# Kernel tuning notes

Measured on AMD Instinct MI355X. Metric: run time of the kernel, lower is better.

Reference implementation:

```python
import jax, jax.numpy as jnp
import numpy as np

B, T, N = 128, 20, 49
VOCAB, EMB, HDIM, VDIM, ATT = 10000, 512, 1024, 512, 512
LN_EPS = 1e-5


def _layer_norm(x, g, b):
    mu = x.mean(-1, keepdims=True)
    var = ((x - mu) ** 2).mean(-1, keepdims=True)
    return (x - mu) * jax.lax.rsqrt(var + LN_EPS) * g + b


def _lstm_cell(x, h, c, Wih, Whh, bih, bhh):
    gates = x @ Wih.T + h @ Whh.T + bih + bhh  # [B, 4H]
    i, f, g, o = jnp.split(gates, 4, axis=-1)  # torch LSTMCell gate order
    c_new = jax.nn.sigmoid(f) * c + jax.nn.sigmoid(i) * jnp.tanh(g)
    h_new = jax.nn.sigmoid(o) * jnp.tanh(c_new)
    return h_new, c_new


def setup_inputs() -> dict:
    key = jax.random.key(0)
    ks = jax.random.split(key, 16)
    w = lambda k, shape: (jax.random.normal(k, shape, jnp.float32) * 0.02)
    embed_W = w(ks[2], (VOCAB, EMB)).at[0].set(0.0)  # padding_idx=0 row is zeros
    return dict(
        V=jax.random.normal(ks[0], (B, N, VDIM), jnp.float32),
        y=jax.random.randint(ks[1], (B, T), 0, VOCAB),
        embed_W=embed_W,
        Vp_W=w(ks[3], (HDIM, VDIM)), Vp_b=jnp.zeros((HDIM,), jnp.float32),
        attW=w(ks[4], (ATT, HDIM)), attU=w(ks[5], (ATT, HDIM)), attv=w(ks[6], (1, ATT)),
        l1_Wih=w(ks[7], (4 * HDIM, EMB + HDIM)), l1_Whh=w(ks[8], (4 * HDIM, HDIM)),
        l1_bih=jnp.zeros((4 * HDIM,), jnp.float32), l1_bhh=jnp.zeros((4 * HDIM,), jnp.float32),
        l2_Wih=w(ks[9], (4 * HDIM, HDIM)), l2_Whh=w(ks[10], (4 * HDIM, HDIM)),
        l2_bih=jnp.zeros((4 * HDIM,), jnp.float32), l2_bhh=jnp.zeros((4 * HDIM,), jnp.float32),
        n1_g=jnp.ones((HDIM,), jnp.float32), n1_b=jnp.zeros((HDIM,), jnp.float32),
        n2_g=jnp.ones((HDIM,), jnp.float32), n2_b=jnp.zeros((HDIM,), jnp.float32),
        ih_W=w(ks[11], (HDIM, HDIM)), ih_b=jnp.zeros((HDIM,), jnp.float32),
        ic_W=w(ks[12], (HDIM, HDIM)), ic_b=jnp.zeros((HDIM,), jnp.float32),
        proj_W=w(ks[13], (EMB, HDIM)),
    )


def reference(V, y, embed_W, Vp_W, Vp_b, attW, attU, attv,
              l1_Wih, l1_Whh, l1_bih, l1_bhh,
              l2_Wih, l2_Whh, l2_bih, l2_bhh,
              n1_g, n1_b, n2_g, n2_b,
              ih_W, ih_b, ic_W, ic_b, proj_W):
    Vp = V @ Vp_W.T + Vp_b                      # [B, N, H]
    feat_mean = Vp.mean(1)                      # [B, H]
    h1 = jnp.tanh(feat_mean @ ih_W.T + ih_b)
    c1 = jnp.tanh(feat_mean @ ic_W.T + ic_b)
    h2 = jnp.zeros_like(h1)
    c2 = jnp.zeros_like(c1)

    Uv = Vp @ attU.T                            # [B, N, ATT] (hoisted out of loop)
    emb_y = embed_W[y]                          # [B, T, EMB]
    xs = jnp.swapaxes(emb_y[:, :-1], 0, 1)      # [T-1, B, EMB]

    def step(carry, x_t):
        h1, c1, h2, c2 = carry
        # additive attention (dropout is identity in eval)
        e = jnp.tanh((h2 @ attW.T)[:, None, :] + Uv) @ attv[0]   # [B, N]
        a = jax.nn.softmax(e, axis=1)
        ctx = jnp.einsum('bn,bnh->bh', a, Vp)
        h1n, c1n = _lstm_cell(jnp.concatenate([x_t, ctx], -1), h1, c1,
                              l1_Wih, l1_Whh, l1_bih, l1_bhh)
        h1n = _layer_norm(h1n, n1_g, n1_b)
        h2n, c2n = _lstm_cell(h1n, h2, c2, l2_Wih, l2_Whh, l2_bih, l2_bhh)
        h2n = _layer_norm(h2n, n2_g, n2_b)
        logit = (h2n @ proj_W.T) @ embed_W.T    # [B, VOCAB]
        return (h1n, c1n, h2n, c2n), logit

    _, logits = jax.lax.scan(step, (h1, c1, h2, c2), xs)
    return jnp.swapaxes(logits, 0, 1)           # [B, T-1, VOCAB]
```

## Files before the change

kernel.cpp:

```cpp
#include <hip/hip_runtime.h>
#include <hip/hip_bf16.h>

#define TSTEPS 19

typedef short bf16x8 __attribute__((ext_vector_type(8)));
typedef short bf16x4 __attribute__((ext_vector_type(4)));
typedef float f32x4 __attribute__((ext_vector_type(4)));

__device__ __forceinline__ f32x4 mfma_bf16(bf16x8 a, bf16x8 b, f32x4 c) {
    return __builtin_amdgcn_mfma_f32_16x16x32_bf16(a, b, c, 0, 0, 0);
}
__device__ __forceinline__ short f2b(float f) {
    union { float f; unsigned u; } v; v.f = f;
    unsigned r = v.u + 0x7fffu + ((v.u >> 16) & 1u);
    return (short)(r >> 16);
}
__device__ __forceinline__ float b2f(short s) {
    union { unsigned u; float f; } v; v.u = ((unsigned)(unsigned short)s) << 16;
    return v.f;
}
__device__ __forceinline__ float sigm(float x) { return 1.f / (1.f + __expf(-x)); }
__device__ __forceinline__ float tanhfast(float x) { return 1.f - 2.f / (__expf(2.f * x) + 1.f); }

__global__ __launch_bounds__(256) void k_convert(
    const float* __restrict__ l1_Wih, const float* __restrict__ l1_Whh,
    const float* __restrict__ l2_Wih, const float* __restrict__ l2_Whh,
    const float* __restrict__ embed_W, const float* __restrict__ proj_W,
    const float* __restrict__ attW, const float* __restrict__ ih_W,
    const float* __restrict__ ic_W, const float* __restrict__ Vp_W,
    const float* __restrict__ attU, const float* __restrict__ V,
    const int* __restrict__ y, const float* __restrict__ n1g,
    const float* __restrict__ n2g,
    short* __restrict__ l1h, short* __restrict__ l1l,
    short* __restrict__ l2h, short* __restrict__ l2l,
    short* __restrict__ embB, short* __restrict__ pa, short* __restrict__ ihic,
    short* __restrict__ VpWh, short* __restrict__ VpWl, short* __restrict__ attUb,
    short* __restrict__ Vbh, short* __restrict__ Vbl, short* __restrict__ xall) {
    const int N1 = 4096 * 2560, N2 = 4096 * 2048, N3 = 10000 * 512, N4 = 1024 * 1024,
              N5 = 2048 * 1024, N6 = 1024 * 512, N7 = 512 * 1024, N8 = 128 * 49 * 512,
              N9 = 19 * 128 * 512;
    const int total4 = (N1 + N2 + N3 + N4 + N5 + N6 + N7 + N8 + N9) >> 2;
    int stride = gridDim.x * blockDim.x;
    for (int g = blockIdx.x * blockDim.x + threadIdx.x; g < total4; g += stride) {
        int e = g << 2;
        if (e < N1) {
            int n = e / 2560, k = e - n * 2560;
            f32x4 v;
            if (k < 1536) {
                v = *(const f32x4*)(l1_Wih + (size_t)n * 1536 + k);
            } else {
                f32x4 w = *(const f32x4*)(l1_Whh + (size_t)n * 1024 + (k - 1536));
                f32x4 gg = *(const f32x4*)(n1g + (k - 1536));
#pragma unroll
                for (int j = 0; j < 4; j++) v[j] = gg[j] * w[j];
            }
            bf16x4 hi, lo;
#pragma unroll
            for (int j = 0; j < 4; j++) { hi[j] = f2b(v[j]); lo[j] = f2b(v[j] - b2f(hi[j])); }
            *(bf16x4*)(l1h + e) = hi; *(bf16x4*)(l1l + e) = lo; continue;
        }
        e -= N1;
        if (e < N2) {
            int n = e >> 11, k = e & 2047;
            f32x4 w, gg;
            if (k < 1024) {
                w = *(const f32x4*)(l2_Wih + (size_t)n * 1024 + k);
                gg = *(const f32x4*)(n1g + k);
            } else {
                w = *(const f32x4*)(l2_Whh + (size_t)n * 1024 + (k - 1024));
                gg = *(const f32x4*)(n2g + (k - 1024));
            }
            bf16x4 hi, lo;
#pragma unroll
            for (int j = 0; j < 4; j++) {
                float v = gg[j] * w[j];
                hi[j] = f2b(v); lo[j] = f2b(v - b2f(hi[j]));
            }
            *(bf16x4*)(l2h + e) = hi; *(bf16x4*)(l2l + e) = lo; continue;
        }
        e -= N2;
        if (e < N3) {
            f32x4 v = *(const f32x4*)(embed_W + e);
            bf16x4 o;
#pragma unroll
            for (int j = 0; j < 4; j++) o[j] = f2b(v[j]);
            *(bf16x4*)(embB + e) = o; continue;
        }
        e -= N3;
        if (e < N4) {
            int n = e >> 10, k = e & 1023;
            f32x4 w = (n < 512) ? *(const f32x4*)(proj_W + (size_t)n * 1024 + k)
                                : *(const f32x4*)(attW + (size_t)(n - 512) * 1024 + k);
            f32x4 gg = *(const f32x4*)(n2g + k);
            bf16x4 o;
#pragma unroll
            for (int j = 0; j < 4; j++) o[j] = f2b(gg[j] * w[j]);
            *(bf16x4*)(pa + e) = o; continue;
        }
        e -= N4;
        if (e < N5) {
            int n = e >> 10, k = e & 1023;
            f32x4 w = (n < 1024) ? *(const f32x4*)(ih_W + (size_t)n * 1024 + k)
                                 : *(const f32x4*)(ic_W + (size_t)(n - 1024) * 1024 + k);
            bf16x4 o;
#pragma unroll
            for (int j = 0; j < 4; j++) o[j] = f2b(w[j]);
            *(bf16x4*)(ihic + e) = o; continue;
        }
        e -= N5;
        if (e < N6) {
            f32x4 v = *(const f32x4*)(Vp_W + e);
            bf16x4 hi, lo;
#pragma unroll
            for (int j = 0; j < 4; j++) { hi[j] = f2b(v[j]); lo[j] = f2b(v[j] - b2f(hi[j])); }
            *(bf16x4*)(VpWh + e) = hi; *(bf16x4*)(VpWl + e) = lo; continue;
        }
        e -= N6;
        if (e < N7) {
            f32x4 v = *(const f32x4*)(attU + e);
            bf16x4 o;
#pragma unroll
            for (int j = 0; j < 4; j++) o[j] = f2b(v[j]);
            *(bf16x4*)(attUb + e) = o; continue;
        }
        e -= N7;
        if (e < N8) {
            f32x4 v = *(const f32x4*)(V + e);
            bf16x4 hi, lo;
#pragma unroll
            for (int j = 0; j < 4; j++) { hi[j] = f2b(v[j]); lo[j] = f2b(v[j] - b2f(hi[j])); }
            *(bf16x4*)(Vbh + e) = hi; *(bf16x4*)(Vbl + e) = lo; continue;
        }
        e -= N8;
        {
            int t = e >> 16; int r = e & 65535;
            int b = r >> 9, k = r & 511;
            int idx = y[b * 20 + t];
            f32x4 v = *(const f32x4*)(embed_W + (size_t)idx * 512 + k);
            bf16x4 o;
#pragma unroll
            for (int j = 0; j < 4; j++) o[j] = f2b(v[j]);
            *(bf16x4*)(xall + e) = o;
        }
    }
}

__global__ __launch_bounds__(256) void k_corr(
    const float* __restrict__ l1_Whh, const float* __restrict__ l2_Wih,
    const float* __restrict__ l2_Whh, const float* __restrict__ proj_W,
    const float* __restrict__ attW,
    const float* __restrict__ n1g, const float* __restrict__ n1b,
    const float* __restrict__ n2g, const float* __restrict__ n2b,
    float* __restrict__ wg1, float* __restrict__ wb1,
    float* __restrict__ wg2a, float* __restrict__ wb2a,
    float* __restrict__ wg2b, float* __restrict__ wb2b,
    float* __restrict__ wgp, float* __restrict__ wbp) {
    int w = (blockIdx.x * 256 + threadIdx.x) >> 6;
    int lane = threadIdx.x & 63;
    if (w >= 13312) return;
    const float* row; const float* g; const float* b; float* og; float* ob;
    if (w < 4096)       { row = l1_Whh + (size_t)w * 1024; g = n1g; b = n1b; og = wg1 + w; ob = wb1 + w; }
    else if (w < 8192)  { int j = w - 4096; row = l2_Wih + (size_t)j * 1024; g = n1g; b = n1b; og = wg2a + j; ob = wb2a + j; }
    else if (w < 12288) { int j = w - 8192; row = l2_Whh + (size_t)j * 1024; g = n2g; b = n2b; og = wg2b + j; ob = wb2b + j; }
    else                { int j = w - 12288;
                          row = (j < 512) ? proj_W + (size_t)j * 1024 : attW + (size_t)(j - 512) * 1024;
                          g = n2g; b = n2b; og = wgp + j; ob = wbp + j; }
    float sg = 0.f, sb = 0.f;
    for (int k = lane; k < 1024; k += 64) { float wv = row[k]; sg += g[k] * wv; sb += b[k] * wv; }
#pragma unroll
    for (int o = 1; o < 64; o <<= 1) { sg += __shfl_xor(sg, o); sb += __shfl_xor(sb, o); }
    if (lane == 0) { *og = sg; *ob = sb; }
}

__device__ __forceinline__ void gemm_core(const short* __restrict__ A, int lda,
                                          const short* __restrict__ Bm, int ldb,
                                          int mb, int n0, int K, int Nlim,
                                          f32x4 acc[2][4]) {
    int lane = threadIdx.x & 63, wave = threadIdx.x >> 6;
    int col = lane & 15, quad = lane >> 4;
    const short* a0p = A + (size_t)(mb + wave * 32 + col) * lda + quad * 8;
    const short* a1p = a0p + (size_t)16 * lda;
    const short* bp[4];
#pragma unroll
    for (int s = 0; s < 4; s++) {
        int n = n0 + s * 16 + col;
        if (n >= Nlim) n = 0;
        bp[s] = Bm + (size_t)n * ldb + quad * 8;
    }
    for (int kb = 0; kb < K; kb += 32) {
        bf16x8 a0 = *(const bf16x8*)(a0p + kb);
        bf16x8 a1 = *(const bf16x8*)(a1p + kb);
#pragma unroll
        for (int s = 0; s < 4; s++) {
            bf16x8 b = *(const bf16x8*)(bp[s] + kb);
            acc[0][s] = mfma_bf16(a0, b, acc[0][s]);
            acc[1][s] = mfma_bf16(a1, b, acc[1][s]);
        }
    }
}

__global__ __launch_bounds__(256) void k_gemm_vp(const short* __restrict__ Ah,
                                                 const short* __restrict__ Al,
                                                 const short* __restrict__ Bh,
                                                 const short* __restrict__ Bl,
                                                 const float* __restrict__ Vp_b,
                                                 short* __restrict__ Vph,
                                                 short* __restrict__ Vpl) {
    __shared__ alignas(16) short Bs[2 * 64 * 256];
    char* Bsb = (char*)Bs;
    int tid = threadIdx.x, lane = tid & 63, wave = tid >> 6, col = lane & 15, quad = lane >> 4;
    int mb = blockIdx.y * 128, n0 = blockIdx.x * 64;
    f32x4 acc[2][4] = {};
    const short* ah0 = Ah + (size_t)(mb + wave * 32 + col) * 512 + quad * 8;
    const short* al0 = Al + (size_t)(mb + wave * 32 + col) * 512 + quad * 8;
    const short* ah1 = ah0 + 16 * 512; const short* al1 = al0 + 16 * 512;
#pragma unroll
    for (int ph = 0; ph < 2; ph++) {
        int kbase = ph * 256;
        __syncthreads();
#pragma unroll
        for (int i = 0; i < 8; i++) {
            int r = i * 8 + wave * 2 + (lane >> 5);
            int n = n0 + r;
            int e = (lane & 31) * 8;
            bf16x8 vh = *(const bf16x8*)(Bh + (size_t)n * 512 + kbase + e);
            bf16x8 vl = *(const bf16x8*)(Bl + (size_t)n * 512 + kbase + e);
            int wo = r * 512 + ((e * 2) ^ ((r & 7) << 4));
            *(bf16x8*)(Bsb + wo) = vh;
            *(bf16x8*)(Bsb + 32768 + wo) = vl;
        }
        __syncthreads();
        for (int kb = 0; kb < 256; kb += 32) {
            bf16x8 h0 = *(const bf16x8*)(ah0 + kbase + kb), l0 = *(const bf16x8*)(al0 + kbase + kb);
            bf16x8 h1 = *(const bf16x8*)(ah1 + kbase + kb), l1 = *(const bf16x8*)(al1 + kbase + kb);
#pragma unroll
            for (int s = 0; s < 4; s++) {
                int r = s * 16 + col;
                int off = r * 512 + ((quad * 16 + kb * 2) ^ ((r & 7) << 4));
                bf16x8 wh = *(const bf16x8*)(Bsb + off);
                bf16x8 wl = *(const bf16x8*)(Bsb + 32768 + off);
                acc[0][s] = mfma_bf16(h0, wh, acc[0][s]);
                acc[0][s] = mfma_bf16(l0, wh, acc[0][s]);
                acc[0][s] = mfma_bf16(h0, wl, acc[0][s]);
                acc[1][s] = mfma_bf16(h1, wh, acc[1][s]);
                acc[1][s] = mfma_bf16(l1, wh, acc[1][s]);
                acc[1][s] = mfma_bf16(h1, wl, acc[1][s]);
            }
        }
    }
#pragma unroll
    for (int i = 0; i < 2; i++)
#pragma unroll
        for (int s = 0; s < 4; s++) {
            int n = n0 + s * 16 + col;
            float bias = Vp_b[n];
#pragma unroll
            for (int r = 0; r < 4; r++) {
                int m = mb + wave * 32 + i * 16 + quad * 4 + r;
                float v = acc[i][s][r] + bias;
                short hi = f2b(v);
                Vph[(size_t)m * 1024 + n] = hi;
                Vpl[(size_t)m * 1024 + n] = f2b(v - b2f(hi));
            }
        }
}

__global__ __launch_bounds__(256) void k_gemm_uv(const short* __restrict__ Vph,
                                                 const short* __restrict__ Vpl,
                                                 const short* __restrict__ attUb,
                                                 short* __restrict__ Uv) {
    __shared__ alignas(16) short Bs[64 * 512];
    char* Bsb = (char*)Bs;
    int tid = threadIdx.x, lane = tid & 63, wave = tid >> 6, col = lane & 15, quad = lane >> 4;
    int mb = blockIdx.y * 128, n0 = blockIdx.x * 64;
    f32x4 acc[2][4] = {};
    const short* ah0 = Vph + (size_t)(mb + wave * 32 + col) * 1024 + quad * 8;
    const short* al0 = Vpl + (size_t)(mb + wave * 32 + col) * 1024 + quad * 8;
    const short* ah1 = ah0 + 16 * 1024; const short* al1 = al0 + 16 * 1024;
#pragma unroll
    for (int ph = 0; ph < 2; ph++) {
        int kbase = ph * 512;
        __syncthreads();
#pragma unroll
        for (int i = 0; i < 16; i++) {
            int r = i * 4 + wave;
            int n = n0 + r;
            int e = lane * 8;
            bf16x8 v = *(const bf16x8*)(attUb + (size_t)n * 1024 + kbase + e);
            *(bf16x8*)(Bsb + r * 1024 + ((e * 2) ^ ((r & 7) << 4))) = v;
        }
        __syncthreads();
        for (int kb = 0; kb < 512; kb += 32) {
            bf16x8 h0 = *(const bf16x8*)(ah0 + kbase + kb), l0 = *(const bf16x8*)(al0 + kbase + kb);
            bf16x8 h1 = *(const bf16x8*)(ah1 + kbase + kb), l1 = *(const bf16x8*)(al1 + kbase + kb);
#pragma unroll
            for (int s = 0; s < 4; s++) {
                int r = s * 16 + col;
                bf16x8 b = *(const bf16x8*)(Bsb + r * 1024 + ((quad * 16 + kb * 2) ^ ((r & 7) << 4)));
                acc[0][s] = mfma_bf16(h0, b, acc[0][s]);
                acc[0][s] = mfma_bf16(l0, b, acc[0][s]);
                acc[1][s] = mfma_bf16(h1, b, acc[1][s]);
                acc[1][s] = mfma_bf16(l1, b, acc[1][s]);
            }
        }
    }
#pragma unroll
    for (int i = 0; i < 2; i++)
#pragma unroll
        for (int s = 0; s < 4; s++) {
            int n = n0 + s * 16 + col;
#pragma unroll
            for (int r = 0; r < 4; r++) {
                int m = mb + wave * 32 + i * 16 + quad * 4 + r;
                Uv[(size_t)m * 512 + n] = f2b(acc[i][s][r]);
            }
        }
}

__global__ __launch_bounds__(256) void k_gemm_xpart(const short* __restrict__ xall,
                                                    const short* __restrict__ l1h,
                                                    float* __restrict__ xpart) {
    f32x4 acc[2][4] = {};
    int mb = blockIdx.y * 128, n0 = blockIdx.x * 64;
    gemm_core(xall, 512, l1h, 2560, mb, n0, 512, 1 << 30, acc);
    int lane = threadIdx.x & 63, wave = threadIdx.x >> 6, col = lane & 15, quad = lane >> 4;
#pragma unroll
    for (int i = 0; i < 2; i++)
#pragma unroll
        for (int s = 0; s < 4; s++) {
            int n = n0 + s * 16 + col;
#pragma unroll
            for (int r = 0; r < 4; r++) {
                int m = mb + wave * 32 + i * 16 + quad * 4 + r;
                xpart[(size_t)m * 4096 + n] = acc[i][s][r];
            }
        }
}

__global__ __launch_bounds__(256) void k_feat(const short* __restrict__ Vph,
                                              const short* __restrict__ Vpl,
                                              short* __restrict__ feat,
                                              float* __restrict__ c2,
                                              short* __restrict__ h2h1,
                                              short* __restrict__ h2l1,
                                              float* __restrict__ st1,
                                              float* __restrict__ st2) {
    int b = blockIdx.x, tid = threadIdx.x;
    int h0 = tid * 4;
    float acc[4] = {0.f, 0.f, 0.f, 0.f};
    for (int n = 0; n < 49; n++) {
        bf16x4 vh = *(const bf16x4*)(Vph + ((size_t)b * 49 + n) * 1024 + h0);
        bf16x4 vl = *(const bf16x4*)(Vpl + ((size_t)b * 49 + n) * 1024 + h0);
#pragma unroll
        for (int j = 0; j < 4; j++) acc[j] += b2f(vh[j]) + b2f(vl[j]);
    }
    bf16x4 o;
#pragma unroll
    for (int j = 0; j < 4; j++) o[j] = f2b(acc[j] * (1.f / 49.f));
    *(bf16x4*)(feat + (size_t)b * 1024 + h0) = o;
#pragma unroll
    for (int j = 0; j < 4; j++) {
        c2[(size_t)b * 1024 + h0 + j] = 0.f;
        h2h1[(size_t)b * 1024 + h0 + j] = 0;
        h2l1[(size_t)b * 1024 + h0 + j] = 0;
    }
    if (tid == 0) {
        st1[(128 + b) * 2] = 0.f; st1[(128 + b) * 2 + 1] = 1.f;
        st2[(128 + b) * 2] = 0.f; st2[(128 + b) * 2 + 1] = 1.f;
    }
}

__global__ __launch_bounds__(256) void k_gemm_h1c1(const short* __restrict__ feat,
                                                   const short* __restrict__ ihic,
                                                   const float* __restrict__ ih_b,
                                                   const float* __restrict__ ic_b,
                                                   short* __restrict__ h1h1,
                                                   short* __restrict__ h1l1,
                                                   float* __restrict__ c1) {
    f32x4 acc[2][4] = {};
    int n0 = blockIdx.y * 64;
    gemm_core(feat, 1024, ihic, 1024, 0, n0, 1024, 1 << 30, acc);
    int lane = threadIdx.x & 63, wave = threadIdx.x >> 6, col = lane & 15, quad = lane >> 4;
#pragma unroll
    for (int i = 0; i < 2; i++)
#pragma unroll
        for (int s = 0; s < 4; s++) {
            int n = n0 + s * 16 + col;
#pragma unroll
            for (int r = 0; r < 4; r++) {
                int m = wave * 32 + i * 16 + quad * 4 + r;
                float v = acc[i][s][r];
                if (n < 1024) {
                    float t = tanhfast(v + ih_b[n]);
                    short hi = f2b(t);
                    h1h1[(size_t)m * 1024 + n] = hi;
                    h1l1[(size_t)m * 1024 + n] = f2b(t - b2f(hi));
                } else {
                    c1[(size_t)m * 1024 + (n - 1024)] = tanhfast(v + ic_b[n - 1024]);
                }
            }
        }
}

__global__ __launch_bounds__(256) void k_attn(
        int t,
        const float* __restrict__ pproj,
        const float* __restrict__ st2p,
        const float* __restrict__ wgp, const float* __restrict__ wbp,
        short* __restrict__ pbuf_prev,
        const short* __restrict__ Uv,
        const float* __restrict__ attv, const short* __restrict__ Vph,
        const short* __restrict__ Vpl,
        short* __restrict__ ctxh, short* __restrict__ ctxl) {
    int b = blockIdx.x, tid = threadIdx.x;
    int lane = tid & 63, wave = tid >> 6;
    __shared__ float shW[512];
    __shared__ float se[49], sa[49];
    if (t == 0) {
        shW[tid] = 0.f; shW[tid + 256] = 0.f;
    } else {
        float mu = st2p[b * 2], rs = st2p[b * 2 + 1];
        int n4 = tid * 4;
        f32x4 p0 = *(const f32x4*)(pproj + (size_t)b * 1024 + n4);
        f32x4 p1 = *(const f32x4*)(pproj + 131072 + (size_t)b * 1024 + n4);
        f32x4 wb = *(const f32x4*)(wbp + n4);
        f32x4 wg = *(const f32x4*)(wgp + n4);
        float v[4];
#pragma unroll
        for (int j = 0; j < 4; j++) v[j] = rs * (p0[j] + p1[j]) + wb[j] - rs * mu * wg[j];
        if (n4 < 512) {
            bf16x4 o;
#pragma unroll
            for (int j = 0; j < 4; j++) o[j] = f2b(v[j]);
            *(bf16x4*)(pbuf_prev + (size_t)b * 512 + n4) = o;
        } else {
#pragma unroll
            for (int j = 0; j < 4; j++) shW[n4 - 512 + j] = v[j];
        }
    }
    __syncthreads();
    for (int n = wave; n < 49; n += 4) {
        const float* hw = shW + lane * 8;
        const short* uv = Uv + ((size_t)b * 49 + n) * 512 + lane * 8;
        const float* av = attv + lane * 8;
        bf16x8 u8 = *(const bf16x8*)uv;
        float part = 0.f;
#pragma unroll
        for (int j = 0; j < 8; j++) part += tanhfast(hw[j] + b2f(u8[j])) * av[j];
#pragma unroll
        for (int o = 1; o < 64; o <<= 1) part += __shfl_xor(part, o);
        if (lane == 0) se[n] = part;
    }
    __syncthreads();
    if (wave == 0) {
        float v = (lane < 49) ? se[lane] : -1e30f;
        float mx = v;
#pragma unroll
        for (int o = 1; o < 64; o <<= 1) mx = fmaxf(mx, __shfl_xor(mx, o));
        float p = (lane < 49) ? __expf(v - mx) : 0.f;
        float s = p;
#pragma unroll
        for (int o = 1; o < 64; o <<= 1) s += __shfl_xor(s, o);
        if (lane < 49) sa[lane] = p / s;
    }
    __syncthreads();
    {
        int h0 = tid * 4;
        float acc[4] = {0.f, 0.f, 0.f, 0.f};
        for (int n = 0; n < 49; n++) {
            float wgt = sa[n];
            bf16x4 vh = *(const bf16x4*)(Vph + ((size_t)b * 49 + n) * 1024 + h0);
            bf16x4 vl = *(const bf16x4*)(Vpl + ((size_t)b * 49 + n) * 1024 + h0);
#pragma unroll
            for (int j = 0; j < 4; j++) acc[j] += wgt * (b2f(vh[j]) + b2f(vl[j]));
        }
        bf16x4 oh, ol;
#pragma unroll
        for (int j = 0; j < 4; j++) {
            short hi = f2b(acc[j]); oh[j] = hi; ol[j] = f2b(acc[j] - b2f(hi));
        }
        *(bf16x4*)(ctxh + (size_t)b * 1024 + h0) = oh;
        *(bf16x4*)(ctxl + (size_t)b * 1024 + h0) = ol;
    }
}

__global__ __launch_bounds__(256) void k_lstm1_mm(
        const short* __restrict__ ctxh, const short* __restrict__ ctxl,
        const short* __restrict__ h1hp, const short* __restrict__ h1lp,
        const short* __restrict__ l1h, const short* __restrict__ l1l,
        float* __restrict__ part) {
    __shared__ alignas(16) short Bs[2 * 64 * 256];
    char* Bsb = (char*)Bs;
    int bn = blockIdx.x, bk = blockIdx.y;
    int tid = threadIdx.x, lane = tid & 63, wave = tid >> 6, col = lane & 15, quad = lane >> 4;
    int n0 = bn * 64;
    int kw0 = 512 + bk * 256;
#pragma unroll
    for (int i = 0; i < 8; i++) {
        int r = i * 8 + wave * 2 + (lane >> 5);
        int e = (lane & 31) * 8;
        size_t src = (size_t)(n0 + r) * 2560 + kw0 + e;
        bf16x8 vh = *(const bf16x8*)(l1h + src);
        bf16x8 vl = *(const bf16x8*)(l1l + src);
        int wo = r * 512 + ((e * 2) ^ ((r & 7) << 4));
        *(bf16x8*)(Bsb + wo) = vh;
        *(bf16x8*)(Bsb + 32768 + wo) = vl;
    }
    __syncthreads();
    f32x4 acc[2][4] = {};
    int r0 = wave * 32 + col;
    const short* Ah = (bk < 4) ? ctxh : h1hp;
    const short* Al = (bk < 4) ? ctxl : h1lp;
    int ko = (bk & 3) * 256;
    const short* a0h = Ah + (size_t)r0 * 1024 + ko + quad * 8;
    const short* a0l = Al + (size_t)r0 * 1024 + ko + quad * 8;
    const short* a1h = a0h + 16 * 1024; const short* a1l = a0l + 16 * 1024;
    for (int kb = 0; kb < 256; kb += 32) {
        bf16x8 h0 = *(const bf16x8*)(a0h + kb), l0 = *(const bf16x8*)(a0l + kb);
        bf16x8 h1 = *(const bf16x8*)(a1h + kb), l1 = *(const bf16x8*)(a1l + kb);
#pragma unroll
        for (int s = 0; s < 4; s++) {
            int r = s * 16 + col;
            int off = r * 512 + ((quad * 16 + kb * 2) ^ ((r & 7) << 4));
            bf16x8 wh = *(const bf16x8*)(Bsb + off);
            bf16x8 wl = *(const bf16x8*)(Bsb + 32768 + off);
            acc[0][s] = mfma_bf16(h0, wh, acc[0][s]);
            acc[0][s] = mfma_bf16(l0, wh, acc[0][s]);
            acc[0][s] = mfma_bf16(h0, wl, acc[0][s]);
            acc[1][s] = mfma_bf16(h1, wh, acc[1][s]);
            acc[1][s] = mfma_bf16(l1, wh, acc[1][s]);
            acc[1][s] = mfma_bf16(h1, wl, acc[1][s]);
        }
    }
#pragma unroll
    for (int i = 0; i < 2; i++)
#pragma unroll
        for (int s = 0; s < 4; s++)
#pragma unroll
            for (int r = 0; r < 4; r++) {
                int m = wave * 32 + i * 16 + quad * 4 + r;
                part[((size_t)bk * 128 + m) * 4096 + n0 + s * 16 + col] = acc[i][s][r];
            }
}

__global__ __launch_bounds__(256) void k_red1(const float* __restrict__ part,
        const float* __restrict__ xpart_t,
        const float* __restrict__ st_prev,
        const float* __restrict__ wg1, const float* __restrict__ wb1,
        const float* __restrict__ bih, const float* __restrict__ bhh,
        float* __restrict__ c1, short* __restrict__ h1hc, short* __restrict__ h1lc,
        float* __restrict__ st_cur) {
    int m = blockIdx.x, tid = threadIdx.x;
    float mu_p = st_prev[m * 2], rs_p = st_prev[m * 2 + 1];
    const size_t SB = 128UL * 4096;
    int h = tid * 4;
    float pre[4][4];
#pragma unroll
    for (int g = 0; g < 4; g++) {
        int n = g * 1024 + h;
        size_t base = (size_t)m * 4096 + n;
        f32x4 pA = *(const f32x4*)(xpart_t + base);
        f32x4 pB = {};
#pragma unroll
        for (int q = 0; q < 4; q++) {
            f32x4 pa_ = *(const f32x4*)(part + q * SB + base);
            f32x4 pb_ = *(const f32x4*)(part + (q + 4) * SB + base);
#pragma unroll
            for (int j = 0; j < 4; j++) { pA[j] += pa_[j]; pB[j] += pb_[j]; }
        }
        f32x4 wb = *(const f32x4*)(wb1 + n);
        f32x4 wg = *(const f32x4*)(wg1 + n);
        f32x4 bi = *(const f32x4*)(bih + n);
        f32x4 bh = *(const f32x4*)(bhh + n);
#pragma unroll
        for (int j = 0; j < 4; j++)
            pre[g][j] = pA[j] + rs_p * pB[j] + wb[j] - rs_p * mu_p * wg[j] + bi[j] + bh[j];
    }
    size_t idx = (size_t)m * 1024 + h;
    f32x4 cv = *(const f32x4*)(c1 + idx);
    f32x4 cn_v; bf16x4 oh, ol;
    float s1 = 0.f, s2 = 0.f;
#pragma unroll
    for (int j = 0; j < 4; j++) {
        float cn = sigm(pre[1][j]) * cv[j] + sigm(pre[0][j]) * tanhfast(pre[2][j]);
        float hn = sigm(pre[3][j]) * tanhfast(cn);
        cn_v[j] = cn;
        short hi = f2b(hn); oh[j] = hi; ol[j] = f2b(hn - b2f(hi));
        s1 += hn; s2 += hn * hn;
    }
    *(f32x4*)(c1 + idx) = cn_v;
    *(bf16x4*)(h1hc + idx) = oh;
    *(bf16x4*)(h1lc + idx) = ol;
    __shared__ float red[8];
    int lane = tid & 63, wave = tid >> 6;
#pragma unroll
    for (int o = 1; o < 64; o <<= 1) { s1 += __shfl_xor(s1, o); s2 += __shfl_xor(s2, o); }
    if (lane == 0) { red[wave * 2] = s1; red[wave * 2 + 1] = s2; }
    __syncthreads();
    if (tid == 0) {
        float S1 = red[0] + red[2] + red[4] + red[6];
        float S2 = red[1] + red[3] + red[5] + red[7];
        float mu = S1 * (1.f / 1024.f);
        float var = S2 * (1.f / 1024.f) - mu * mu;
        st_cur[m * 2] = mu; st_cur[m * 2 + 1] = rsqrtf(var + 1e-5f);
    }
}

__global__ __launch_bounds__(256) void k_lstm2_mm(
        const short* __restrict__ h1hc, const short* __restrict__ h1lc,
        const short* __restrict__ h2hp, const short* __restrict__ h2lp,
        const short* __restrict__ l2h, const short* __restrict__ l2l,
        float* __restrict__ part) {
    __shared__ alignas(16) short Bs[2 * 64 * 256];
    char* Bsb = (char*)Bs;
    int bn = blockIdx.x, bk = blockIdx.y;
    int tid = threadIdx.x, lane = tid & 63, wave = tid >> 6, col = lane & 15, quad = lane >> 4;
    int n0 = bn * 64;
    int kw0 = bk * 256;
#pragma unroll
    for (int i = 0; i < 8; i++) {
        int r = i * 8 + wave * 2 + (lane >> 5);
        int e = (lane & 31) * 8;
        size_t src = (size_t)(n0 + r) * 2048 + kw0 + e;
        bf16x8 vh = *(const bf16x8*)(l2h + src);
        bf16x8 vl = *(const bf16x8*)(l2l + src);
        int wo = r * 512 + ((e * 2) ^ ((r & 7) << 4));
        *(bf16x8*)(Bsb + wo) = vh;
        *(bf16x8*)(Bsb + 32768 + wo) = vl;
    }
    __syncthreads();
    f32x4 acc[2][4] = {};
    int r0 = wave * 32 + col;
    const short* Ah = (bk < 4) ? h1hc : h2hp;
    const short* Al = (bk < 4) ? h1lc : h2lp;
    int ko = (bk & 3) * 256;
    const short* a0h = Ah + (size_t)r0 * 1024 + ko + quad * 8;
    const short* a0l = Al + (size_t)r0 * 1024 + ko + quad * 8;
    const short* a1h = a0h + 16 * 1024; const short* a1l = a0l + 16 * 1024;
    for (int kb = 0; kb < 256; kb += 32) {
        bf16x8 h0 = *(const bf16x8*)(a0h + kb), l0 = *(const bf16x8*)(a0l + kb);
        bf16x8 h1 = *(const bf16x8*)(a1h + kb), l1 = *(const bf16x8*)(a1l + kb);
#pragma unroll
        for (int s = 0; s < 4; s++) {
            int r = s * 16 + col;
            int off = r * 512 + ((quad * 16 + kb * 2) ^ ((r & 7) << 4));
            bf16x8 wh = *(const bf16x8*)(Bsb + off);
            bf16x8 wl = *(const bf16x8*)(Bsb + 32768 + off);
            acc[0][s] = mfma_bf16(h0, wh, acc[0][s]);
            acc[0][s] = mfma_bf16(l0, wh, acc[0][s]);
            acc[0][s] = mfma_bf16(h0, wl, acc[0][s]);
            acc[1][s] = mfma_bf16(h1, wh, acc[1][s]);
            acc[1][s] = mfma_bf16(l1, wh, acc[1][s]);
            acc[1][s] = mfma_bf16(h1, wl, acc[1][s]);
        }
    }
#pragma unroll
    for (int i = 0; i < 2; i++)
#pragma unroll
        for (int s = 0; s < 4; s++)
#pragma unroll
            for (int r = 0; r < 4; r++) {
                int m = wave * 32 + i * 16 + quad * 4 + r;
                part[((size_t)bk * 128 + m) * 4096 + n0 + s * 16 + col] = acc[i][s][r];
            }
}

__global__ __launch_bounds__(256) void k_red2(const float* __restrict__ part,
        const float* __restrict__ stA, const float* __restrict__ stB,
        const float* __restrict__ wg2a, const float* __restrict__ wb2a,
        const float* __restrict__ wg2b, const float* __restrict__ wb2b,
        const float* __restrict__ bih, const float* __restrict__ bhh,
        float* __restrict__ c2, short* __restrict__ h2hc, short* __restrict__ h2lc,
        float* __restrict__ st_cur) {
    int m = blockIdx.x, tid = threadIdx.x;
    float mu1 = stA[m * 2], rs1 = stA[m * 2 + 1];
    float mu2 = stB[m * 2], rs2 = stB[m * 2 + 1];
    const size_t SB = 128UL * 4096;
    int h = tid * 4;
    float pre[4][4];
#pragma unroll
    for (int g = 0; g < 4; g++) {
        int n = g * 1024 + h;
        size_t base = (size_t)m * 4096 + n;
        f32x4 pA = {}, pB = {};
#pragma unroll
        for (int q = 0; q < 4; q++) {
            f32x4 pa_ = *(const f32x4*)(part + q * SB + base);
            f32x4 pb_ = *(const f32x4*)(part + (q + 4) * SB + base);
#pragma unroll
            for (int j = 0; j < 4; j++) { pA[j] += pa_[j]; pB[j] += pb_[j]; }
        }
        f32x4 wba = *(const f32x4*)(wb2a + n);
        f32x4 wga = *(const f32x4*)(wg2a + n);
        f32x4 wbb = *(const f32x4*)(wb2b + n);
        f32x4 wgb = *(const f32x4*)(wg2b + n);
        f32x4 bi = *(const f32x4*)(bih + n);
        f32x4 bh = *(const f32x4*)(bhh + n);
#pragma unroll
        for (int j = 0; j < 4; j++)
            pre[g][j] = rs1 * pA[j] + rs2 * pB[j]
                        + wba[j] - rs1 * mu1 * wga[j]
                        + wbb[j] - rs2 * mu2 * wgb[j] + bi[j] + bh[j];
    }
    size_t idx = (size_t)m * 1024 + h;
    f32x4 cv = *(const f32x4*)(c2 + idx);
    f32x4 cn_v; bf16x4 oh, ol;
    float s1 = 0.f, s2 = 0.f;
#pragma unroll
    for (int j = 0; j < 4; j++) {
        float cn = sigm(pre[1][j]) * cv[j] + sigm(pre[0][j]) * tanhfast(pre[2][j]);
        float hn = sigm(pre[3][j]) * tanhfast(cn);
        cn_v[j] = cn;
        short hi = f2b(hn); oh[j] = hi; ol[j] = f2b(hn - b2f(hi));
        s1 += hn; s2 += hn * hn;
    }
    *(f32x4*)(c2 + idx) = cn_v;
    *(bf16x4*)(h2hc + idx) = oh;
    *(bf16x4*)(h2lc + idx) = ol;
    __shared__ float red[8];
    int lane = tid & 63, wave = tid >> 6;
#pragma unroll
    for (int o = 1; o < 64; o <<= 1) { s1 += __shfl_xor(s1, o); s2 += __shfl_xor(s2, o); }
    if (lane == 0) { red[wave * 2] = s1; red[wave * 2 + 1] = s2; }
    __syncthreads();
    if (tid == 0) {
        float S1 = red[0] + red[2] + red[4] + red[6];
        float S2 = red[1] + red[3] + red[5] + red[7];
        float mu = S1 * (1.f / 1024.f);
        float var = S2 * (1.f / 1024.f) - mu * mu;
        st_cur[m * 2] = mu; st_cur[m * 2 + 1] = rsqrtf(var + 1e-5f);
    }
}

__global__ __launch_bounds__(256) void k_projatt(
        const short* __restrict__ h2hc, const short* __restrict__ h2lc,
        const short* __restrict__ pa,
        float* __restrict__ pproj) {
    int nt = blockIdx.x, mh = blockIdx.y, kc = blockIdx.z;
    int tid = threadIdx.x, lane = tid & 63, wave = tid >> 6, col = lane & 15, quad = lane >> 4;
    int arow = mh * 64 + wave * 16 + col;
    int n = nt * 16 + col;
    int k0 = kc * 512;
    f32x4 acc = {};
    const short* bp = pa + (size_t)n * 1024 + k0 + quad * 8;
    const short* ah = h2hc + (size_t)arow * 1024 + k0 + quad * 8;
    const short* al = h2lc + (size_t)arow * 1024 + k0 + quad * 8;
    for (int kb = 0; kb < 512; kb += 32) {
        bf16x8 xh = *(const bf16x8*)(ah + kb);
        bf16x8 xl = *(const bf16x8*)(al + kb);
        bf16x8 b = *(const bf16x8*)(bp + kb);
        acc = mfma_bf16(xh, b, acc);
        acc = mfma_bf16(xl, b, acc);
    }
#pragma unroll
    for (int r = 0; r < 4; r++) {
        int m = mh * 64 + wave * 16 + quad * 4 + r;
        pproj[(size_t)kc * 131072 + (size_t)m * 1024 + nt * 16 + col] = acc[r];
    }
}

__global__ __launch_bounds__(256) void k_pbuf(const float* __restrict__ pproj,
        const float* __restrict__ st2c,
        const float* __restrict__ wgp, const float* __restrict__ wbp,
        short* __restrict__ pbuf) {
    int b = blockIdx.x, tid = threadIdx.x;
    float mu = st2c[b * 2], rs = st2c[b * 2 + 1];
#pragma unroll
    for (int j = 0; j < 2; j++) {
        int n = tid * 2 + j;
        float v = rs * (pproj[(size_t)b * 1024 + n] + pproj[131072 + (size_t)b * 1024 + n])
                  + wbp[n] - rs * mu * wgp[n];
        pbuf[(size_t)b * 512 + n] = f2b(v);
    }
}

__global__ __launch_bounds__(256) void k_logits_all(const short* __restrict__ pbuf_all,
                                                    const short* __restrict__ embB,
                                                    float* __restrict__ out) {
    const int NWG = 157 * 19, Q = NWG / 8, R8 = NWG % 8;
    int orig = blockIdx.x;
    int xcd = orig & 7, local = orig >> 3;
    int wid = (xcd < R8 ? xcd * (Q + 1) : R8 * (Q + 1) + (xcd - R8) * Q) + local;
    int nt = wid / 19, t = wid - nt * 19;
    int n0 = nt * 64;
    __shared__ alignas(16) short Bs[64 * 512];
    char* Bsb = (char*)Bs;
    int tid = threadIdx.x, lane = tid & 63, wave = tid >> 6;
#pragma unroll
    for (int i = 0; i < 16; i++) {
        int r = i * 4 + wave;
        int n = n0 + r; if (n >= 10000) n = 0;
        bf16x8 v = *(const bf16x8*)(embB + (size_t)n * 512 + lane * 8);
        *(bf16x8*)(Bsb + r * 1024 + ((lane * 16) ^ ((r & 7) << 4))) = v;
    }
    __syncthreads();
    int col = lane & 15, quad = lane >> 4;
    f32x4 acc[2][4] = {};
    const short* A = pbuf_all + (size_t)t * 128 * 512;
    const short* a0p = A + (size_t)(wave * 32 + col) * 512 + quad * 8;
    const short* a1p = a0p + 16 * 512;
    int rbase[4], rkey[4];
#pragma unroll
    for (int s = 0; s < 4; s++) {
        int r = s * 16 + col;
        rbase[s] = r * 1024;
        rkey[s] = (r & 7) << 4;
    }
#pragma unroll 4
    for (int kb = 0; kb < 512; kb += 32) {
        bf16x8 a0 = *(const bf16x8*)(a0p + kb);
        bf16x8 a1 = *(const bf16x8*)(a1p + kb);
#pragma unroll
        for (int s = 0; s < 4; s++) {
            bf16x8 bfrag = *(const bf16x8*)(Bsb + rbase[s] + ((quad * 16 + kb * 2) ^ rkey[s]));
            acc[0][s] = mfma_bf16(a0, bfrag, acc[0][s]);
            acc[1][s] = mfma_bf16(a1, bfrag, acc[1][s]);
        }
    }
#pragma unroll
    for (int i = 0; i < 2; i++)
#pragma unroll
        for (int s = 0; s < 4; s++) {
            int n = n0 + s * 16 + col;
            if (n >= 10000) continue;
#pragma unroll
            for (int r = 0; r < 4; r++) {
                int m = wave * 32 + i * 16 + quad * 4 + r;
                out[((size_t)m * 19 + t) * 10000 + n] = acc[i][s][r];
            }
        }
}

extern "C" void kernel_launch(void* const* d_in, const int* in_sizes, int n_in,
                              void* d_out, int out_size, void* d_ws, size_t ws_size,
                              hipStream_t stream) {
    const float* V = (const float*)d_in[0];
    const int* y = (const int*)d_in[1];
    const float* embed_W = (const float*)d_in[2];
    const float* Vp_W = (const float*)d_in[3];
    const float* Vp_b = (const float*)d_in[4];
    const float* attW = (const float*)d_in[5];
    const float* attU = (const float*)d_in[6];
    const float* attv = (const float*)d_in[7];
    const float* l1_Wih = (const float*)d_in[8];
    const float* l1_Whh = (const float*)d_in[9];
    const float* l1_bih = (const float*)d_in[10];
    const float* l1_bhh = (const float*)d_in[11];
    const float* l2_Wih = (const float*)d_in[12];
    const float* l2_Whh = (const float*)d_in[13];
    const float* l2_bih = (const float*)d_in[14];
    const float* l2_bhh = (const float*)d_in[15];
    const float* n1g = (const float*)d_in[16];
    const float* n1b = (const float*)d_in[17];
    const float* n2g = (const float*)d_in[18];
    const float* n2b = (const float*)d_in[19];
    const float* ih_W = (const float*)d_in[20];
    const float* ih_b = (const float*)d_in[21];
    const float* ic_W = (const float*)d_in[22];
    const float* ic_b = (const float*)d_in[23];
    const float* proj_W = (const float*)d_in[24];
    float* out = (float*)d_out;
    (void)in_sizes; (void)n_in; (void)out_size;

    char* wsp = (char*)d_ws;
    size_t off = 0;
    auto alloc = [&](size_t bytes) -> void* {
        void* p = wsp + off;
        off += (bytes + 255) & ~(size_t)255;
        return p;
    };
    short* l1h  = (short*)alloc(4096UL * 2560 * 2);
    short* l1l  = (short*)alloc(4096UL * 2560 * 2);
    short* l2h  = (short*)alloc(4096UL * 2048 * 2);
    short* l2l  = (short*)alloc(4096UL * 2048 * 2);
    short* embB = (short*)alloc(10000UL * 512 * 2);
    short* pa   = (short*)alloc(1024UL * 1024 * 2);
    short* ihic = (short*)alloc(2048UL * 1024 * 2);
    short* VpWh = (short*)alloc(1024UL * 512 * 2);
    short* VpWl = (short*)alloc(1024UL * 512 * 2);
    short* attUb= (short*)alloc(512UL * 1024 * 2);
    short* Vbh  = (short*)alloc(128UL * 49 * 512 * 2);
    short* Vbl  = (short*)alloc(128UL * 49 * 512 * 2);
    short* xall = (short*)alloc(19UL * 128 * 512 * 2);
    short* Vph  = (short*)alloc(6272UL * 1024 * 2);
    short* Vpl  = (short*)alloc(6272UL * 1024 * 2);
    short* Uv   = (short*)alloc(6272UL * 512 * 2);
    short* feat = (short*)alloc(128UL * 1024 * 2);
    short* ctxh = (short*)alloc(128UL * 1024 * 2);
    short* ctxl = (short*)alloc(128UL * 1024 * 2);
    short* h1h  = (short*)alloc(2UL * 128 * 1024 * 2);
    short* h1l  = (short*)alloc(2UL * 128 * 1024 * 2);
    short* h2h  = (short*)alloc(2UL * 128 * 1024 * 2);
    short* h2l  = (short*)alloc(2UL * 128 * 1024 * 2);
    short* pbuf_all = (short*)alloc(19UL * 128 * 512 * 2);
    float* c1   = (float*)alloc(128UL * 1024 * 4);
    float* c2   = (float*)alloc(128UL * 1024 * 4);
    float* st1  = (float*)alloc(2UL * 128 * 2 * 4);
    float* st2  = (float*)alloc(2UL * 128 * 2 * 4);
    float* pmm  = (float*)alloc(8UL * 128 * 4096 * 4);
    float* pproj= (float*)alloc(2UL * 128 * 1024 * 4);
    float* xpart= (float*)alloc(2432UL * 4096 * 4);
    float* wg1  = (float*)alloc(4096UL * 4);
    float* wb1  = (float*)alloc(4096UL * 4);
    float* wg2a = (float*)alloc(4096UL * 4);
    float* wb2a = (float*)alloc(4096UL * 4);
    float* wg2b = (float*)alloc(4096UL * 4);
    float* wb2b = (float*)alloc(4096UL * 4);
    float* wgp  = (float*)alloc(1024UL * 4);
    float* wbp  = (float*)alloc(1024UL * 4);
    if (off > ws_size) return;

    const size_t HB = 128UL * 1024;
    const size_t SB2 = 128UL * 2;

    k_convert<<<2048, 256, 0, stream>>>(l1_Wih, l1_Whh, l2_Wih, l2_Whh, embed_W, proj_W,
                                        attW, ih_W, ic_W, Vp_W, attU, V, y, n1g, n2g,
                                        l1h, l1l, l2h, l2l, embB, pa, ihic,
                                        VpWh, VpWl, attUb, Vbh, Vbl, xall);
    k_corr<<<3328, 256, 0, stream>>>(l1_Whh, l2_Wih, l2_Whh, proj_W, attW,
                                     n1g, n1b, n2g, n2b,
                                     wg1, wb1, wg2a, wb2a, wg2b, wb2b, wgp, wbp);
    k_gemm_vp<<<dim3(16, 49), 256, 0, stream>>>(Vbh, Vbl, VpWh, VpWl, Vp_b, Vph, Vpl);
    k_gemm_xpart<<<dim3(64, 19), 256, 0, stream>>>(xall, l1h, xpart);
    k_feat<<<128, 256, 0, stream>>>(Vph, Vpl, feat, c2, h2h + HB, h2l + HB, st1, st2);
    k_gemm_h1c1<<<dim3(1, 32), 256, 0, stream>>>(feat, ihic, ih_b, ic_b,
                                                 h1h + HB, h1l + HB, c1);
    k_gemm_uv<<<dim3(8, 49), 256, 0, stream>>>(Vph, Vpl, attUb, Uv);

    for (int t = 0; t < TSTEPS; t++) {
        int cur = t & 1, prev = cur ^ 1;
        short* pbuf_prev = pbuf_all + (size_t)(t > 0 ? t - 1 : 0) * 128 * 512;
        k_attn<<<128, 256, 0, stream>>>(t, pproj, st2 + prev * SB2, wgp, wbp,
                                        pbuf_prev, Uv, attv, Vph, Vpl, ctxh, ctxl);
        k_lstm1_mm<<<dim3(64, 8), 256, 0, stream>>>(ctxh, ctxl,
                                                    h1h + prev * HB, h1l + prev * HB,
                                                    l1h, l1l, pmm);
        k_red1<<<128, 256, 0, stream>>>(pmm, xpart + (size_t)t * 128 * 4096,
                                        st1 + prev * SB2, wg1, wb1,
                                        l1_bih, l1_bhh, c1,
                                        h1h + cur * HB, h1l + cur * HB, st1 + cur * SB2);
        k_lstm2_mm<<<dim3(64, 8), 256, 0, stream>>>(h1h + cur * HB, h1l + cur * HB,
                                                    h2h + prev * HB, h2l + prev * HB,
                                                    l2h, l2l, pmm);
        k_red2<<<128, 256, 0, stream>>>(pmm, st1 + cur * SB2, st2 + prev * SB2,
                                        wg2a, wb2a, wg2b, wb2b, l2_bih, l2_bhh, c2,
                                        h2h + cur * HB, h2l + cur * HB, st2 + cur * SB2);
        k_projatt<<<dim3(64, 2, 2), 256, 0, stream>>>(h2h + cur * HB, h2l + cur * HB,
                                                      pa, pproj);
    }
    k_pbuf<<<128, 256, 0, stream>>>(pproj, st2, wgp, wbp,
                                    pbuf_all + 18UL * 128 * 512);
    k_logits_all<<<dim3(157 * 19), 256, 0, stream>>>(pbuf_all, embB, out);
}
```

Before: 1.944 ms.

## Fuse attention projection into red2 and batch output projection after loop

Removes the per-step k_projatt launch. red2 now computes the attention query projection (h2 @ attW-based rows of pa) itself, using a scalar dot product from shared memory, and writes hW for the next step's attention. The output-projection half is deferred: all h2 states and LN stats are kept across the 19 steps and projected in one batched MFMA GEMM after the loop. This saves 19 launches and moves half the projection work off the sequential critical path. In exchange, red2 does a serial 1024-long dot per output with non-MFMA math and uses only the high bf16 part of the weights with fp32 h.

```diff
diff --git a/kernel.cpp b/kernel.cpp
--- a/kernel.cpp
+++ b/kernel.cpp
@@ -340,9 +340,10 @@
 __global__ __launch_bounds__(256) void k_feat(const short* __restrict__ Vph,
                                               const short* __restrict__ Vpl,
                                               short* __restrict__ feat,
+                                              float* __restrict__ hW,
                                               float* __restrict__ c2,
-                                              short* __restrict__ h2h1,
-                                              short* __restrict__ h2l1,
+                                              short* __restrict__ h2h0,
+                                              short* __restrict__ h2l0,
                                               float* __restrict__ st1,
                                               float* __restrict__ st2) {
     int b = blockIdx.x, tid = threadIdx.x;
@@ -358,15 +359,17 @@
 #pragma unroll
     for (int j = 0; j < 4; j++) o[j] = f2b(acc[j] * (1.f / 49.f));
     *(bf16x4*)(feat + (size_t)b * 1024 + h0) = o;
+    hW[(size_t)b * 512 + tid * 2] = 0.f;
+    hW[(size_t)b * 512 + tid * 2 + 1] = 0.f;
 #pragma unroll
     for (int j = 0; j < 4; j++) {
         c2[(size_t)b * 1024 + h0 + j] = 0.f;
-        h2h1[(size_t)b * 1024 + h0 + j] = 0;
-        h2l1[(size_t)b * 1024 + h0 + j] = 0;
+        h2h0[(size_t)b * 1024 + h0 + j] = 0;
+        h2l0[(size_t)b * 1024 + h0 + j] = 0;
     }
     if (tid == 0) {
         st1[(128 + b) * 2] = 0.f; st1[(128 + b) * 2 + 1] = 1.f;
-        st2[(128 + b) * 2] = 0.f; st2[(128 + b) * 2 + 1] = 1.f;
+        st2[b * 2] = 0.f; st2[b * 2 + 1] = 1.f;
     }
 }
 
@@ -403,11 +406,7 @@
 }
 
 __global__ __launch_bounds__(256) void k_attn(
-        int t,
-        const float* __restrict__ pproj,
-        const float* __restrict__ st2p,
-        const float* __restrict__ wgp, const float* __restrict__ wbp,
-        short* __restrict__ pbuf_prev,
+        const float* __restrict__ hW,
         const short* __restrict__ Uv,
         const float* __restrict__ attv, const short* __restrict__ Vph,
         const short* __restrict__ Vpl,
@@ -416,28 +415,8 @@
     int lane = tid & 63, wave = tid >> 6;
     __shared__ float shW[512];
     __shared__ float se[49], sa[49];
-    if (t == 0) {
-        shW[tid] = 0.f; shW[tid + 256] = 0.f;
-    } else {
-        float mu = st2p[b * 2], rs = st2p[b * 2 + 1];
-        int n4 = tid * 4;
-        f32x4 p0 = *(const f32x4*)(pproj + (size_t)b * 1024 + n4);
-        f32x4 p1 = *(const f32x4*)(pproj + 131072 + (size_t)b * 1024 + n4);
-        f32x4 wb = *(const f32x4*)(wbp + n4);
-        f32x4 wg = *(const f32x4*)(wgp + n4);
-        float v[4];
-#pragma unroll
-        for (int j = 0; j < 4; j++) v[j] = rs * (p0[j] + p1[j]) + wb[j] - rs * mu * wg[j];
-        if (n4 < 512) {
-            bf16x4 o;
-#pragma unroll
-            for (int j = 0; j < 4; j++) o[j] = f2b(v[j]);
-            *(bf16x4*)(pbuf_prev + (size_t)b * 512 + n4) = o;
-        } else {
-#pragma unroll
-            for (int j = 0; j < 4; j++) shW[n4 - 512 + j] = v[j];
-        }
-    }
+    shW[tid * 2]     = hW[(size_t)b * 512 + tid * 2];
+    shW[tid * 2 + 1] = hW[(size_t)b * 512 + tid * 2 + 1];
     __syncthreads();
     for (int n = wave; n < 49; n += 4) {
         const float* hw = shW + lane * 8;
@@ -670,8 +649,10 @@
         const float* __restrict__ wg2a, const float* __restrict__ wb2a,
         const float* __restrict__ wg2b, const float* __restrict__ wb2b,
         const float* __restrict__ bih, const float* __restrict__ bhh,
+        const short* __restrict__ pa,
+        const float* __restrict__ wgp, const float* __restrict__ wbp,
         float* __restrict__ c2, short* __restrict__ h2hc, short* __restrict__ h2lc,
-        float* __restrict__ st_cur) {
+        float* __restrict__ st_cur, float* __restrict__ hW) {
     int m = blockIdx.x, tid = threadIdx.x;
     float mu1 = stA[m * 2], rs1 = stA[m * 2 + 1];
     float mu2 = stB[m * 2], rs2 = stB[m * 2 + 1];
@@ -704,20 +685,23 @@
     }
     size_t idx = (size_t)m * 1024 + h;
     f32x4 cv = *(const f32x4*)(c2 + idx);
-    f32x4 cn_v; bf16x4 oh, ol;
+    f32x4 cn_v, hn_v; bf16x4 oh, ol;
     float s1 = 0.f, s2 = 0.f;
 #pragma unroll
     for (int j = 0; j < 4; j++) {
         float cn = sigm(pre[1][j]) * cv[j] + sigm(pre[0][j]) * tanhfast(pre[2][j]);
         float hn = sigm(pre[3][j]) * tanhfast(cn);
-        cn_v[j] = cn;
+        cn_v[j] = cn; hn_v[j] = hn;
         short hi = f2b(hn); oh[j] = hi; ol[j] = f2b(hn - b2f(hi));
         s1 += hn; s2 += hn * hn;
     }
     *(f32x4*)(c2 + idx) = cn_v;
     *(bf16x4*)(h2hc + idx) = oh;
     *(bf16x4*)(h2lc + idx) = ol;
+    __shared__ float sh2[1024];
     __shared__ float red[8];
+    __shared__ float sstat[2];
+    *(f32x4*)(sh2 + h) = hn_v;
     int lane = tid & 63, wave = tid >> 6;
 #pragma unroll
     for (int o = 1; o < 64; o <<= 1) { s1 += __shfl_xor(s1, o); s2 += __shfl_xor(s2, o); }
@@ -728,50 +712,82 @@
         float S2 = red[1] + red[3] + red[5] + red[7];
         float mu = S1 * (1.f / 1024.f);
         float var = S2 * (1.f / 1024.f) - mu * mu;
-        st_cur[m * 2] = mu; st_cur[m * 2 + 1] = rsqrtf(var + 1e-5f);
-    }
-}
-
-__global__ __launch_bounds__(256) void k_projatt(
-        const short* __restrict__ h2hc, const short* __restrict__ h2lc,
-        const short* __restrict__ pa,
-        float* __restrict__ pproj) {
-    int nt = blockIdx.x, mh = blockIdx.y, kc = blockIdx.z;
+        float rs = rsqrtf(var + 1e-5f);
+        st_cur[m * 2] = mu; st_cur[m * 2 + 1] = rs;
+        sstat[0] = mu; sstat[1] = rs;
+    }
+    __syncthreads();
+    float muc = sstat[0], rsc = sstat[1];
+#pragma unroll
+    for (int jo = 0; jo < 2; jo++) {
+        int n = tid * 2 + jo;
+        const short* pr = pa + (size_t)(512 + n) * 1024;
+        float acc2 = 0.f;
+        for (int k = 0; k < 1024; k += 8) {
+            bf16x8 w = *(const bf16x8*)(pr + k);
+#pragma unroll
+            for (int j = 0; j < 8; j++) acc2 += sh2[k + j] * b2f(w[j]);
+        }
+        hW[(size_t)m * 512 + n] = rsc * acc2 + wbp[512 + n] - rsc * muc * wgp[512 + n];
+    }
+}
+
+__global__ __launch_bounds__(256) void k_pbuf_all(
+        const short* __restrict__ h2all_h, const short* __restrict__ h2all_l,
+        const float* __restrict__ st2all, const short* __restrict__ pa,
+        const float* __restrict__ wgp, const float* __restrict__ wbp,
+        short* __restrict__ pbuf_all) {
+    __shared__ alignas(16) short Bs[64 * 512];
+    char* Bsb = (char*)Bs;
     int tid = threadIdx.x, lane = tid & 63, wave = tid >> 6, col = lane & 15, quad = lane >> 4;
-    int arow = mh * 64 + wave * 16 + col;
-    int n = nt * 16 + col;
-    int k0 = kc * 512;
-    f32x4 acc = {};
-    const short* bp = pa + (size_t)n * 1024 + k0 + quad * 8;
-    const short* ah = h2hc + (size_t)arow * 1024 + k0 + quad * 8;
-    const short* al = h2lc + (size_t)arow * 1024 + k0 + quad * 8;
-    for (int kb = 0; kb < 512; kb += 32) {
-        bf16x8 xh = *(const bf16x8*)(ah + kb);
-        bf16x8 xl = *(const bf16x8*)(al + kb);
-        bf16x8 b = *(const bf16x8*)(bp + kb);
-        acc = mfma_bf16(xh, b, acc);
-        acc = mfma_bf16(xl, b, acc);
-    }
-#pragma unroll
-    for (int r = 0; r < 4; r++) {
-        int m = mh * 64 + wave * 16 + quad * 4 + r;
-        pproj[(size_t)kc * 131072 + (size_t)m * 1024 + nt * 16 + col] = acc[r];
-    }
-}
-
-__global__ __launch_bounds__(256) void k_pbuf(const float* __restrict__ pproj,
-        const float* __restrict__ st2c,
-        const float* __restrict__ wgp, const float* __restrict__ wbp,
-        short* __restrict__ pbuf) {
-    int b = blockIdx.x, tid = threadIdx.x;
-    float mu = st2c[b * 2], rs = st2c[b * 2 + 1];
-#pragma unroll
-    for (int j = 0; j < 2; j++) {
-        int n = tid * 2 + j;
-        float v = rs * (pproj[(size_t)b * 1024 + n] + pproj[131072 + (size_t)b * 1024 + n])
-                  + wbp[n] - rs * mu * wgp[n];
-        pbuf[(size_t)b * 512 + n] = f2b(v);
-    }
+    int n0 = blockIdx.x * 64, t = blockIdx.y;
+    const short* Ah = h2all_h + (size_t)(t + 1) * 131072;
+    const short* Al = h2all_l + (size_t)(t + 1) * 131072;
+    f32x4 acc[2][4] = {};
+    const short* ah0 = Ah + (size_t)(wave * 32 + col) * 1024 + quad * 8;
+    const short* al0 = Al + (size_t)(wave * 32 + col) * 1024 + quad * 8;
+    const short* ah1 = ah0 + 16 * 1024; const short* al1 = al0 + 16 * 1024;
+#pragma unroll
+    for (int ph = 0; ph < 2; ph++) {
+        int kbase = ph * 512;
+        __syncthreads();
+#pragma unroll
+        for (int i = 0; i < 16; i++) {
+            int r = i * 4 + wave;
+            int n = n0 + r;
+            int e = lane * 8;
+            bf16x8 v = *(const bf16x8*)(pa + (size_t)n * 1024 + kbase + e);
+            *(bf16x8*)(Bsb + r * 1024 + ((e * 2) ^ ((r & 7) << 4))) = v;
+        }
+        __syncthreads();
+        for (int kb = 0; kb < 512; kb += 32) {
+            bf16x8 h0 = *(const bf16x8*)(ah0 + kbase + kb), l0 = *(const bf16x8*)(al0 + kbase + kb);
+            bf16x8 h1 = *(const bf16x8*)(ah1 + kbase + kb), l1 = *(const bf16x8*)(al1 + kbase + kb);
+#pragma unroll
+            for (int s = 0; s < 4; s++) {
+                int r = s * 16 + col;
+                bf16x8 b = *(const bf16x8*)(Bsb + r * 1024 + ((quad * 16 + kb * 2) ^ ((r & 7) << 4)));
+                acc[0][s] = mfma_bf16(h0, b, acc[0][s]);
+                acc[0][s] = mfma_bf16(l0, b, acc[0][s]);
+                acc[1][s] = mfma_bf16(h1, b, acc[1][s]);
+                acc[1][s] = mfma_bf16(l1, b, acc[1][s]);
+            }
+        }
+    }
+#pragma unroll
+    for (int i = 0; i < 2; i++)
+#pragma unroll
+        for (int s = 0; s < 4; s++) {
+            int n = n0 + s * 16 + col;
+#pragma unroll
+            for (int r = 0; r < 4; r++) {
+                int m = wave * 32 + i * 16 + quad * 4 + r;
+                float mu = st2all[((size_t)(t + 1) * 128 + m) * 2];
+                float rs = st2all[((size_t)(t + 1) * 128 + m) * 2 + 1];
+                float v = rs * acc[i][s][r] + wbp[n] - rs * mu * wgp[n];
+                pbuf_all[(size_t)t * 65536 + (size_t)m * 512 + n] = f2b(v);
+            }
+        }
 }
 
 __global__ __launch_bounds__(256) void k_logits_all(const short* __restrict__ pbuf_all,
@@ -890,15 +906,15 @@
     short* ctxl = (short*)alloc(128UL * 1024 * 2);
     short* h1h  = (short*)alloc(2UL * 128 * 1024 * 2);
     short* h1l  = (short*)alloc(2UL * 128 * 1024 * 2);
-    short* h2h  = (short*)alloc(2UL * 128 * 1024 * 2);
-    short* h2l  = (short*)alloc(2UL * 128 * 1024 * 2);
+    short* h2h  = (short*)alloc(20UL * 128 * 1024 * 2);
+    short* h2l  = (short*)alloc(20UL * 128 * 1024 * 2);
     short* pbuf_all = (short*)alloc(19UL * 128 * 512 * 2);
+    float* hW   = (float*)alloc(128UL * 512 * 4);
     float* c1   = (float*)alloc(128UL * 1024 * 4);
     float* c2   = (float*)alloc(128UL * 1024 * 4);
     float* st1  = (float*)alloc(2UL * 128 * 2 * 4);
-    float* st2  = (float*)alloc(2UL * 128 * 2 * 4);
+    float* st2  = (float*)alloc(20UL * 128 * 2 * 4);
     float* pmm  = (float*)alloc(8UL * 128 * 4096 * 4);
-    float* pproj= (float*)alloc(2UL * 128 * 1024 * 4);
     float* xpart= (float*)alloc(2432UL * 4096 * 4);
     float* wg1  = (float*)alloc(4096UL * 4);
     float* wb1  = (float*)alloc(4096UL * 4);
@@ -922,16 +938,14 @@
                                      wg1, wb1, wg2a, wb2a, wg2b, wb2b, wgp, wbp);
     k_gemm_vp<<<dim3(16, 49), 256, 0, stream>>>(Vbh, Vbl, VpWh, VpWl, Vp_b, Vph, Vpl);
     k_gemm_xpart<<<dim3(64, 19), 256, 0, stream>>>(xall, l1h, xpart);
-    k_feat<<<128, 256, 0, stream>>>(Vph, Vpl, feat, c2, h2h + HB, h2l + HB, st1, st2);
+    k_feat<<<128, 256, 0, stream>>>(Vph, Vpl, feat, hW, c2, h2h, h2l, st1, st2);
     k_gemm_h1c1<<<dim3(1, 32), 256, 0, stream>>>(feat, ihic, ih_b, ic_b,
                                                  h1h + HB, h1l + HB, c1);
     k_gemm_uv<<<dim3(8, 49), 256, 0, stream>>>(Vph, Vpl, attUb, Uv);
 
     for (int t = 0; t < TSTEPS; t++) {
         int cur = t & 1, prev = cur ^ 1;
-        short* pbuf_prev = pbuf_all + (size_t)(t > 0 ? t - 1 : 0) * 128 * 512;
-        k_attn<<<128, 256, 0, stream>>>(t, pproj, st2 + prev * SB2, wgp, wbp,
-                                        pbuf_prev, Uv, attv, Vph, Vpl, ctxh, ctxl);
+        k_attn<<<128, 256, 0, stream>>>(hW, Uv, attv, Vph, Vpl, ctxh, ctxl);
         k_lstm1_mm<<<dim3(64, 8), 256, 0, stream>>>(ctxh, ctxl,
                                                     h1h + prev * HB, h1l + prev * HB,
                                                     l1h, l1l, pmm);
@@ -940,15 +954,14 @@
                                         l1_bih, l1_bhh, c1,
                                         h1h + cur * HB, h1l + cur * HB, st1 + cur * SB2);
         k_lstm2_mm<<<dim3(64, 8), 256, 0, stream>>>(h1h + cur * HB, h1l + cur * HB,
-                                                    h2h + prev * HB, h2l + prev * HB,
+                                                    h2h + (size_t)t * HB, h2l + (size_t)t * HB,
                                                     l2h, l2l, pmm);
-        k_red2<<<128, 256, 0, stream>>>(pmm, st1 + cur * SB2, st2 + prev * SB2,
-                                        wg2a, wb2a, wg2b, wb2b, l2_bih, l2_bhh, c2,
-                                        h2h + cur * HB, h2l + cur * HB, st2 + cur * SB2);
-        k_projatt<<<dim3(64, 2, 2), 256, 0, stream>>>(h2h + cur * HB, h2l + cur * HB,
-                                                      pa, pproj);
-    }
-    k_pbuf<<<128, 256, 0, stream>>>(pproj, st2, wgp, wbp,
-                                    pbuf_all + 18UL * 128 * 512);
+        k_red2<<<128, 256, 0, stream>>>(pmm, st1 + cur * SB2, st2 + (size_t)t * SB2,
+                                        wg2a, wb2a, wg2b, wb2b, l2_bih, l2_bhh,
+                                        pa, wgp, wbp, c2,
+                                        h2h + (size_t)(t + 1) * HB, h2l + (size_t)(t + 1) * HB,
+                                        st2 + (size_t)(t + 1) * SB2, hW);
+    }
+    k_pbuf_all<<<dim3(8, 19), 256, 0, stream>>>(h2h, h2l, st2, pa, wgp, wbp, pbuf_all);
     k_logits_all<<<dim3(157 * 19), 256, 0, stream>>>(pbuf_all, embB, out);
 }
```

After: 2.458 ms. 1.26x slower.
